# Kernel tuning notes

Measured on AMD Instinct MI355X. Metric: run time of the kernel, lower is better.

## Reference

```python
import jax, jax.numpy as jnp
import numpy as np

H, HD, C = 16, 64, 64            # num_heads, head_dim, mini_batch_size
BASE_LR = 1.0
EPS = 1e-6                        # ttt LN eps (ln_fwd / ln_fused_l2_bwd)


def _l2norm(x):
    return x / jnp.maximum(jnp.linalg.norm(x, axis=-1, keepdims=True), 1e-12)


def _ln_fwd(x, g, b):
    mu = x.mean(-1, keepdims=True)
    var = x.var(-1, keepdims=True)
    return g * ((x - mu) * jax.lax.rsqrt(var + EPS)) + b


def _ln_l2_bwd(x, tgt, g, b):
    # gradient of ||LN(x)*g+b - tgt||^2 / 2 wrt x
    D = x.shape[-1]
    mu = x.mean(-1, keepdims=True)
    var = x.var(-1, keepdims=True)
    std = jnp.sqrt(var + EPS)
    xh = (x - mu) / std
    gout = (g * xh + b) - tgt
    gxh = gout * g
    return (D * gxh - gxh.sum(-1, keepdims=True) - xh * (gxh * xh).sum(-1, keepdims=True)) / (D * std)


def setup_inputs() -> dict:
    key = jax.random.key(0)
    ks = jax.random.split(key, 12)
    B, L, D = 4, 8192, 1024
    std = 0.02
    return {
        'hidden_states': jax.random.normal(ks[0], (B, L, D), jnp.float32),
        'wq_w': jax.random.normal(ks[1], (D, D), jnp.float32) * std,
        'wq_b': jnp.zeros((D,), jnp.float32),
        'wk_w': jax.random.normal(ks[2], (D, D), jnp.float32) * std,
        'wk_b': jnp.zeros((D,), jnp.float32),
        'wv_w': jax.random.normal(ks[3], (D, D), jnp.float32) * std,
        'wv_b': jnp.zeros((D,), jnp.float32),
        'wo_w': jax.random.normal(ks[4], (D, D), jnp.float32) * std,
        'wo_b': jnp.zeros((D,), jnp.float32),
        'ttt_norm_weight': jnp.ones((H, HD), jnp.float32),
        'ttt_norm_bias': jnp.zeros((H, HD), jnp.float32),
        'ttt_lr_weight': jax.random.normal(ks[5], (H, 1, D), jnp.float32) * std,
        'ttt_lr_bias': jnp.zeros((H, 1), jnp.float32),
        'W1': jax.random.normal(ks[6], (H, HD, HD), jnp.float32) * std,
        'b1': jnp.zeros((H, 1, HD), jnp.float32),
        'post_norm_w': jnp.ones((D,), jnp.float32),
        'post_norm_b': jnp.zeros((D,), jnp.float32),
    }


def _forward(hidden_states, wq_w, wq_b, wk_w, wk_b, wv_w, wv_b, wo_w, wo_b,
             ttt_norm_weight, ttt_norm_bias, ttt_lr_weight, ttt_lr_bias,
             W1, b1, post_norm_w, post_norm_b):
    B, L, D = hidden_states.shape
    NC = L // C
    XQ = (hidden_states @ wq_w.T + wq_b).reshape(B, L, H, HD)
    XK = (hidden_states @ wk_w.T + wk_b).reshape(B, L, H, HD)
    XV = (hidden_states @ wv_w.T + wv_b).reshape(B, L, H, HD)
    XQ = _l2norm(XQ)
    XK = _l2norm(XK)
    # ln_reconstruction_target (uses sample std, ddof=1, eps=1e-5 on std)
    d = XV - XK
    mu = d.mean(-1, keepdims=True)
    sd = d.std(-1, keepdims=True, ddof=1)
    XV = ttt_norm_weight[None, None] * ((d - mu) / (sd + 1e-5)) + ttt_norm_bias[None, None] + XK
    # reshape to mini-batches: [B,H,NC,C,HD]
    Xmb = hidden_states.reshape(B, NC, C, D)
    to_mb = lambda t: t.transpose(0, 2, 1, 3).reshape(B, H, NC, C, HD)
    XQ, XK, XV = to_mb(XQ), to_mb(XK), to_mb(XV)
    # eta: sigmoid lr gate per token, row-broadcast over mini-batch
    ttt_lr = jax.nn.sigmoid(jnp.einsum('bnkc,hdc->bhnkd', Xmb, ttt_lr_weight)
                            + ttt_lr_bias.reshape(1, H, 1, 1, 1))     # [B,H,NC,C,1]
    eta = jnp.swapaxes(ttt_lr, -1, -2) * (BASE_LR / HD / C)           # [B,H,NC,1,C]
    mask = jnp.tril(jnp.ones((C, C), hidden_states.dtype))
    g = ttt_norm_weight[None, :, None, :]
    bta = ttt_norm_bias[None, :, None, :]
    W0 = jnp.broadcast_to(W1[None], (B, H, HD, HD))
    b0 = jnp.broadcast_to(b1[None], (B, H, 1, HD))

    def step(carry, xs):
        W, bvec = carry
        xq, xk, xv, eta_row = xs                      # eta_row: [B,H,1,C]
        Z1 = xk @ W + bvec                            # [B,H,C,HD]
        grad = _ln_l2_bwd(Z1, xv - xk, g, bta)        # [B,H,C,HD]
        Attn = mask * jnp.einsum('bhid,bhjd->bhij', xq, xk)   # [B,H,C,C]
        eta_full = jnp.broadcast_to(eta_row, Attn.shape)      # [B,H,C,C]
        b1_bar = bvec - (mask * eta_full) @ grad              # [B,H,C,HD]
        Z1_bar = xq @ W - (eta_full * Attn) @ grad + b1_bar
        last_eta = eta_full[..., -1, :, None]                 # [B,H,C,1]
        W_new = W - jnp.einsum('bhcd,bhce->bhde', last_eta * xk, grad)
        b_new = bvec - (last_eta * grad).sum(-2, keepdims=True)
        out = xq + _ln_fwd(Z1_bar, g, bta)
        return (W_new, b_new), out

    xs = (jnp.moveaxis(XQ, 2, 0), jnp.moveaxis(XK, 2, 0),
          jnp.moveaxis(XV, 2, 0), jnp.moveaxis(eta, 2, 0))
    _, outs = jax.lax.scan(step, (W0, b0), xs)        # outs: [NC,B,H,C,HD]
    y = jnp.moveaxis(outs, 0, 2).reshape(B, H, L, HD).transpose(0, 2, 1, 3).reshape(B, L, D)
    # post LayerNorm (eps=1e-6) + output projection
    mu2 = y.mean(-1, keepdims=True)
    var2 = y.var(-1, keepdims=True)
    y = post_norm_w * ((y - mu2) * jax.lax.rsqrt(var2 + 1e-6)) + post_norm_b
    return y @ wo_w.T + wo_b


def reference(hidden_states, wq_w, wq_b, wk_w, wk_b, wv_w, wv_b, wo_w, wo_b,
              ttt_norm_weight, ttt_norm_bias, ttt_lr_weight, ttt_lr_bias,
              W1, b1, post_norm_w, post_norm_b):
    return _forward(hidden_states, wq_w, wq_b, wk_w, wk_b, wv_w, wv_b, wo_w, wo_b,
                    ttt_norm_weight, ttt_norm_bias, ttt_lr_weight, ttt_lr_bias,
                    W1, b1, post_norm_w, post_norm_b)
```

## Files before the change

kernel.cpp:

```cpp
#include <hip/hip_runtime.h>


typedef __attribute__((ext_vector_type(8))) short short8;
typedef __attribute__((ext_vector_type(4))) float f32x4;
typedef __attribute__((ext_vector_type(4))) unsigned short us4;

__device__ __forceinline__ float bf2f(unsigned short s) {
  union { unsigned int u; float f; } c;
  c.u = ((unsigned int)s) << 16;
  return c.f;
}
__device__ __forceinline__ unsigned short f2bf(float f) {
  union { float f; unsigned int u; } c;
  c.f = f;
  unsigned int u = c.u;
  return (unsigned short)((u + 0x7FFFu + ((u >> 16) & 1u)) >> 16);
}
__device__ __forceinline__ unsigned cvtpk(float lo, float hi) {
  unsigned r;
  asm("v_cvt_pk_bf16_f32 %0, %1, %2" : "=v"(r) : "v"(lo), "v"(hi));
  return r;
}

__device__ __forceinline__ void gload_lds16(const void* g, void* l) {
  __builtin_amdgcn_global_load_lds(
      (const __attribute__((address_space(1))) unsigned int*)g,
      (__attribute__((address_space(3))) unsigned int*)l, 16, 0, 0);
}

__device__ __forceinline__ float dpp16_sum(float x) {
  int v = __float_as_int(x);
  x += __int_as_float(__builtin_amdgcn_update_dpp(v, v, 0xB1, 0xF, 0xF, true));
  v = __float_as_int(x);
  x += __int_as_float(__builtin_amdgcn_update_dpp(v, v, 0x4E, 0xF, 0xF, true));
  v = __float_as_int(x);
  x += __int_as_float(__builtin_amdgcn_update_dpp(v, v, 0x141, 0xF, 0xF, true));
  v = __float_as_int(x);
  x += __int_as_float(__builtin_amdgcn_update_dpp(v, v, 0x140, 0xF, 0xF, true));
  return x;
}

__device__ __forceinline__ void barrier_fast() {
  __builtin_amdgcn_sched_barrier(0);
  asm volatile("s_waitcnt lgkmcnt(0)" ::: "memory");
  __builtin_amdgcn_s_barrier();
  asm volatile("" ::: "memory");
  __builtin_amdgcn_sched_barrier(0);
}
__device__ __forceinline__ void bar_nowait() {
  __builtin_amdgcn_sched_barrier(0);
  asm volatile("" ::: "memory");
  __builtin_amdgcn_s_barrier();
  asm volatile("" ::: "memory");
  __builtin_amdgcn_sched_barrier(0);
}

__global__ __launch_bounds__(256) void cvt_f32_bf16(
    const float* __restrict__ in, unsigned short* __restrict__ out, long n) {
  long i = ((long)blockIdx.x * 256 + threadIdx.x) * 4;
  if (i + 3 < n) {
    float4 v = *(const float4*)&in[i];
    us4 o = { f2bf(v.x), f2bf(v.y), f2bf(v.z), f2bf(v.w) };
    *(us4*)&out[i] = o;
  }
}

__global__ __launch_bounds__(256) void build_wcat(
    const float* __restrict__ wq, const float* __restrict__ wk,
    const float* __restrict__ wv, const float* __restrict__ lrw,
    const float* __restrict__ wqb, const float* __restrict__ wkb,
    const float* __restrict__ wvb, const float* __restrict__ lrb,
    unsigned short* __restrict__ Wcat, float* __restrict__ biasc) {
  int i = blockIdx.x * 256 + threadIdx.x;
  int row = i >> 10, col = i & 1023;
  int h = row >> 8, o = row & 255;
  float v;
  if (o < 64)        v = wq[(h * 64 + o) * 1024 + col];
  else if (o < 128)  v = wk[(h * 64 + o - 64) * 1024 + col];
  else if (o < 192)  v = wv[(h * 64 + o - 128) * 1024 + col];
  else if (o == 192) v = lrw[h * 1024 + col];
  else               v = 0.f;
  Wcat[i] = f2bf(v);
  if (i < 4096) {
    int hh = i >> 8, oo = i & 255;
    float bv;
    if (oo < 64)        bv = wqb[hh * 64 + oo];
    else if (oo < 128)  bv = wkb[hh * 64 + oo - 64];
    else if (oo < 192)  bv = wvb[hh * 64 + oo - 128];
    else if (oo == 192) bv = lrb[hh];
    else                bv = 0.f;
    biasc[i] = bv;
  }
}

__global__ __launch_bounds__(512, 1) void qkv_scan(
    const unsigned short* __restrict__ A, const unsigned short* __restrict__ B,
    const float* __restrict__ bias, const float* __restrict__ tnw,
    const float* __restrict__ tnb, unsigned short* __restrict__ XQn,
    unsigned short* __restrict__ XKn, unsigned short* __restrict__ TGT,
    float* __restrict__ eta_buf, const float* __restrict__ W1,
    const float* __restrict__ b1, unsigned short* __restrict__ y,
    unsigned int* __restrict__ prog) {
  __shared__ __align__(16) char smem[102912];
  const int tid = threadIdx.x;
  const int lane = tid & 63, wid = tid >> 6;
  const int l15 = lane & 15, lg = lane >> 4;

  if (blockIdx.x >= 64) {
    char* ldsc = smem;
    const int bid2 = blockIdx.x - 64;
    const int w = bid2 >> 6, rem = bid2 & 63, bb = rem >> 4, h = rem & 15;
    const int mprog = bb * 32 + w;
    const long m0 = (long)mprog * 256;
    const long n0 = (long)h * 256;
    const long K = 1024, ldab = 2048;

    const int wm = wid >> 2, wn = wid & 3;
    const int srow = wid * 16 + (lane >> 2);
    const int scol = ((lane & 3) * 16) ^ (((lane >> 3) & 3) << 4);
    const int sdst = wid * 1024;
    const char* Ab = (const char*)A;
    const char* Bb = (const char*)B;
    const int acol = (lg * 16) ^ (((l15 >> 1) & 3) << 4);
    const int aro = (wm * 128 + l15) * 64 + acol;
    const int bro = 16384 + (wn * 64 + l15) * 64 + acol;

#define STG_A(tt, hh, bbu)                                                    \
  gload_lds16(Ab + (size_t)(m0 + (hh) * 128 + srow) * ldab +                  \
                  (size_t)(tt) * 64 + scol,                                   \
              ldsc + (bbu) * 32768 + (hh) * 8192 + sdst)
#define STG_B(tt, hh, bbu)                                                    \
  gload_lds16(Bb + (size_t)(n0 + (hh) * 128 + srow) * ldab +                  \
                  (size_t)(tt) * 64 + scol,                                   \
              ldsc + (bbu) * 32768 + 16384 + (hh) * 8192 + sdst)

    f32x4 acc[8][4];
#pragma unroll
    for (int m = 0; m < 8; ++m)
#pragma unroll
      for (int n = 0; n < 4; ++n) acc[m][n] = (f32x4){0.f, 0.f, 0.f, 0.f};

    const int NT = (int)(K >> 5);
    STG_A(0, 0, 0); STG_A(0, 1, 0); STG_B(0, 0, 0); STG_B(0, 1, 0);
    STG_A(1, 0, 1); STG_A(1, 1, 1); STG_B(1, 0, 1); STG_B(1, 1, 1);
    asm volatile("s_waitcnt vmcnt(4)" ::: "memory");
    bar_nowait();

    int buf = 0, sb = 2;
#pragma unroll 1
    for (int t = 0; t < NT; ++t) {
      if (t + 2 < NT) {
        STG_A(t + 2, 0, sb); STG_A(t + 2, 1, sb);
        STG_B(t + 2, 0, sb); STG_B(t + 2, 1, sb);
      }
      const char* ab = ldsc + buf * 32768 + aro;
      const char* bb2 = ldsc + buf * 32768 + bro;
      short8 av[8], bv[4];
#pragma unroll
      for (int i = 0; i < 8; ++i) av[i] = *(const short8*)(ab + i * 1024);
#pragma unroll
      for (int nf = 0; nf < 4; ++nf) bv[nf] = *(const short8*)(bb2 + nf * 1024);
      __builtin_amdgcn_s_setprio(1);
#pragma unroll
      for (int i = 0; i < 8; ++i)
#pragma unroll
        for (int nf = 0; nf < 4; ++nf)
          acc[i][nf] = __builtin_amdgcn_mfma_f32_16x16x32_bf16(
              av[i], bv[nf], acc[i][nf], 0, 0, 0);
      __builtin_amdgcn_s_setprio(0);
      if (t < NT - 2)
        asm volatile("s_waitcnt vmcnt(4)" ::: "memory");
      else
        asm volatile("s_waitcnt vmcnt(0)" ::: "memory");
      bar_nowait();
      buf = (buf == 2) ? 0 : buf + 1;
      sb = (sb == 2) ? 0 : sb + 1;
    }
#undef STG_A
#undef STG_B

    float bcol[4], twv[4], tbv[4];
#pragma unroll
    for (int nf = 0; nf < 4; ++nf) {
      bcol[nf] = bias[n0 + wn * 64 + nf * 16 + l15];
      twv[nf] = tnw[h * 64 + nf * 16 + l15];
      tbv[nf] = tnb[h * 64 + nf * 16 + l15];
    }
    __syncthreads();
    unsigned short* kn_s = (unsigned short*)smem;

    if (wn == 0) {
#pragma unroll
      for (int mf = 0; mf < 8; ++mf)
#pragma unroll
        for (int j = 0; j < 4; ++j) {
          float v[4], s2 = 0.f;
#pragma unroll
          for (int nf = 0; nf < 4; ++nf) {
            v[nf] = acc[mf][nf][j] + bcol[nf];
            s2 += v[nf] * v[nf];
          }
          s2 = dpp16_sum(s2);
          float rn = 1.f / fmaxf(sqrtf(s2), 1e-12f);
          size_t tt = (size_t)(m0 + wm * 128 + mf * 16 + lg * 4 + j);
#pragma unroll
          for (int nf = 0; nf < 4; ++nf)
            XQn[tt * 1024 + h * 64 + nf * 16 + l15] = f2bf(v[nf] * rn);
        }
    } else if (wn == 1) {
#pragma unroll
      for (int mf = 0; mf < 8; ++mf)
#pragma unroll
        for (int j = 0; j < 4; ++j) {
          float v[4], s2 = 0.f;
#pragma unroll
          for (int nf = 0; nf < 4; ++nf) {
            v[nf] = acc[mf][nf][j] + bcol[nf];
            s2 += v[nf] * v[nf];
          }
          s2 = dpp16_sum(s2);
          float rn = 1.f / fmaxf(sqrtf(s2), 1e-12f);
          size_t tt = (size_t)(m0 + wm * 128 + mf * 16 + lg * 4 + j);
          int lr_ = wm * 128 + mf * 16 + lg * 4 + j;
#pragma unroll
          for (int nf = 0; nf < 4; ++nf) {
            unsigned short kb = f2bf(v[nf] * rn);
            XKn[tt * 1024 + h * 64 + nf * 16 + l15] = kb;
            kn_s[lr_ * 72 + nf * 16 + l15] = kb;
          }
        }
    }
    __syncthreads();
    if (wn == 2) {
#pragma unroll
      for (int mf = 0; mf < 8; ++mf)
#pragma unroll
        for (int j = 0; j < 4; ++j) {
          int lr_ = wm * 128 + mf * 16 + lg * 4 + j;
          float dv[4], s1 = 0.f, s2 = 0.f;
#pragma unroll
          for (int nf = 0; nf < 4; ++nf) {
            float kn = bf2f(kn_s[lr_ * 72 + nf * 16 + l15]);
            dv[nf] = acc[mf][nf][j] + bcol[nf] - kn;
            s1 += dv[nf];
            s2 += dv[nf] * dv[nf];
          }
          s1 = dpp16_sum(s1);
          s2 = dpp16_sum(s2);
          float mu = s1 * 0.015625f;
          float var1 = fmaxf(s2 - 64.f * mu * mu, 0.f) * (1.f / 63.f);
          float rs = 1.f / (sqrtf(var1) + 1e-5f);
          size_t tt = (size_t)(m0 + wm * 128 + mf * 16 + lg * 4 + j);
#pragma unroll
          for (int nf = 0; nf < 4; ++nf)
            TGT[tt * 1024 + h * 64 + nf * 16 + l15] =
                f2bf(twv[nf] * ((dv[nf] - mu) * rs) + tbv[nf]);
        }
    } else if (wn == 3 && l15 == 0) {
#pragma unroll
      for (int mf = 0; mf < 8; ++mf)
#pragma unroll
        for (int j = 0; j < 4; ++j) {
          size_t tt = (size_t)(m0 + wm * 128 + mf * 16 + lg * 4 + j);
          float lgt = acc[mf][0][j] + bcol[0];
          float sig = 1.f / (1.f + expf(-lgt));
          eta_buf[((tt >> 13) * 16 + h) * 8192 + (tt & 8191)] =
              sig * (1.f / 4096.f);
        }
    }
    asm volatile("s_waitcnt vmcnt(0)" ::: "memory");
    __syncthreads();
    if (tid == 0) {
      __threadfence();
      __hip_atomic_fetch_add(&prog[mprog], 1u, __ATOMIC_RELEASE,
                             __HIP_MEMORY_SCOPE_AGENT);
    }
    return;
  }

  unsigned short* xq_s = (unsigned short*)(smem);
  unsigned short* tg_s = (unsigned short*)(smem + 18432);
  unsigned short* xk_s = (unsigned short*)(smem + 36864);
  unsigned short* gc_s = (unsigned short*)(smem + 55296);
  unsigned short* gradT = (unsigned short*)(smem + 64512);
  unsigned short* xkTe = (unsigned short*)(smem + 73728);
  unsigned short* WT_b = (unsigned short*)(smem + 82944);
  float* eta_s = (float*)(smem + 101376);
  float* bpart = (float*)(smem + 101888);

  const int bh = blockIdx.x;
  const int b = bh >> 4, h = bh & 15;
  const bool isA = wid < 4;
  const int q = wid & 3;
  const size_t tokb = (size_t)b * 8192;
  const int col0 = h * 64;
  const int rr_ = q * 16 + (lane >> 3);
  const int c8_ = (lane & 7) * 8;

  short8 pA0[2], pA1[2], pB0[2];
  float peta = 0.f;
  float bstv[4], gwv[4], gbv[4];
  f32x4 Wreg[4];

  if (isA) {
#pragma unroll
    for (int n = 0; n < 4; ++n) {
      int e = n * 16 + l15;
      bstv[n] = b1[h * 64 + e];
      gwv[n] = tnw[h * 64 + e];
      gbv[n] = tnb[h * 64 + e];
    }
  } else {
#pragma unroll
    for (int n = 0; n < 4; ++n)
#pragma unroll
      for (int jj = 0; jj < 4; ++jj) {
        int d = q * 16 + lg * 4 + jj, e = n * 16 + l15;
        float w2 = W1[h * 4096 + d * 64 + e];
        Wreg[n][jj] = w2;
        WT_b[e * 72 + d] = f2bf(w2);
      }
  }
  if (tid == 0) {
    while (__hip_atomic_load(&prog[b << 5], __ATOMIC_ACQUIRE,
                             __HIP_MEMORY_SCOPE_AGENT) < 16u)
      __builtin_amdgcn_s_sleep(16);
  }
  __syncthreads();

  if (isA) {
#pragma unroll
    for (int j = 0; j < 2; ++j) {
      size_t g = (tokb + rr_ + j * 8) * 1024 + col0 + c8_;
      pA0[j] = *(const short8*)&XQn[g];
      pA1[j] = *(const short8*)&TGT[g];
    }
#pragma unroll
    for (int j = 0; j < 2; ++j) {
      int rr = rr_ + j * 8;
      *(short8*)&xq_s[rr * 72 + c8_] = pA0[j];
      *(short8*)&tg_s[rr * 72 + c8_] = pA1[j];
    }
#pragma unroll
    for (int j = 0; j < 2; ++j) {
      size_t g = (tokb + 64 + rr_ + j * 8) * 1024 + col0 + c8_;
      pA0[j] = *(const short8*)&XQn[g];
      pA1[j] = *(const short8*)&TGT[g];
    }
  } else {
#pragma unroll
    for (int j = 0; j < 2; ++j)
      pB0[j] = *(const short8*)&XKn[(tokb + rr_ + j * 8) * 1024 + col0 + c8_];
#pragma unroll
    for (int j = 0; j < 2; ++j)
      *(short8*)&xk_s[(rr_ + j * 8) * 72 + c8_] = pB0[j];
#pragma unroll
    for (int j = 0; j < 2; ++j)
      pB0[j] = *(const short8*)&XKn[(tokb + 64 + rr_ + j * 8) * 1024 + col0 + c8_];
    if (wid == 4) {
      eta_s[lane] = eta_buf[(size_t)bh * 8192 + lane];
      peta = eta_buf[(size_t)bh * 8192 + 64 + lane];
    }
  }
  __syncthreads();

  for (int nc = 0; nc < 128; ++nc) {
    const int p = nc & 1;
    if (nc + 2 < 128 && ((nc + 2) & 3) == 0) {
      if (tid == 0) {
        while (__hip_atomic_load(&prog[(b << 5) + ((nc + 2) >> 2)],
                                 __ATOMIC_ACQUIRE,
                                 __HIP_MEMORY_SCOPE_AGENT) < 16u)
          __builtin_amdgcn_s_sleep(16);
      }
      bar_nowait();
    }
    const unsigned short* WTc = WT_b + p * 4608;
    unsigned short* WTn = WT_b + (p ^ 1) * 4608;
    unsigned short* xqp = xq_s + p * 4608;
    unsigned short* tgp = tg_s + p * 4608;
    unsigned short* xkp = xk_s + p * 4608;
    float* etp = eta_s + p * 64;

    if (isA) {
      if (nc) {
#pragma unroll
        for (int n = 0; n < 4; ++n) {
          int e = n * 16 + l15;
          bstv[n] -= bpart[e] + bpart[64 + e] + bpart[128 + e] + bpart[192 + e];
        }
      }
      if (nc + 1 < 128) {
        unsigned short* xqn = xq_s + (p ^ 1) * 4608;
        unsigned short* tgn = tg_s + (p ^ 1) * 4608;
#pragma unroll
        for (int j = 0; j < 2; ++j) {
          int rr = rr_ + j * 8;
          *(short8*)&xqn[rr * 72 + c8_] = pA0[j];
          *(short8*)&tgn[rr * 72 + c8_] = pA1[j];
        }
      }
      if (nc + 2 < 128) {
#pragma unroll
        for (int j = 0; j < 2; ++j) {
          size_t g = (tokb + (nc + 2) * 64 + rr_ + j * 8) * 1024 + col0 + c8_;
          pA0[j] = *(const short8*)&XQn[g];
          pA1[j] = *(const short8*)&TGT[g];
        }
      }
      f32x4 accZ[4];
#pragma unroll
      for (int n = 0; n < 4; ++n)
        accZ[n] = (f32x4){bstv[n], bstv[n], bstv[n], bstv[n]};
      __builtin_amdgcn_s_setprio(1);
#pragma unroll
      for (int kk = 0; kk < 2; ++kk) {
        const int ko = kk * 32 + lg * 8;
        short8 a_xk = *(const short8*)&xkp[(q * 16 + l15) * 72 + ko];
#pragma unroll
        for (int n = 0; n < 4; ++n) {
          short8 b_w = *(const short8*)&WTc[(n * 16 + l15) * 72 + ko];
          accZ[n] = __builtin_amdgcn_mfma_f32_16x16x32_bf16(a_xk, b_w, accZ[n], 0, 0, 0);
        }
      }
      __builtin_amdgcn_s_setprio(0);
      float grv[4][4];
#pragma unroll
      for (int j = 0; j < 4; ++j) {
        const int r = q * 16 + lg * 4 + j;
        float z[4], s1 = 0.f, s2 = 0.f;
#pragma unroll
        for (int n = 0; n < 4; ++n) {
          z[n] = accZ[n][j];
          s1 += z[n];
          s2 += z[n] * z[n];
        }
        s1 = dpp16_sum(s1);
        s2 = dpp16_sum(s2);
        float mu = s1 * 0.015625f;
        float var = s2 * 0.015625f - mu * mu;
        float rstd = rsqrtf(var + 1e-6f);
        float xh[4], gx[4], s3 = 0.f, s4 = 0.f;
#pragma unroll
        for (int n = 0; n < 4; ++n) {
          xh[n] = (z[n] - mu) * rstd;
          float tg = bf2f(tgp[r * 72 + n * 16 + l15]);
          float go = gwv[n] * xh[n] + gbv[n] - tg;
          gx[n] = go * gwv[n];
          s3 += gx[n];
          s4 += gx[n] * xh[n];
        }
        s3 = dpp16_sum(s3);
        s4 = dpp16_sum(s4);
#pragma unroll
        for (int n = 0; n < 4; ++n)
          grv[n][j] = (64.f * gx[n] - s3 - xh[n] * s4) * rstd * 0.015625f;
      }
#pragma unroll
      for (int n = 0; n < 4; ++n) {
        us4 pk = {f2bf(grv[n][0]), f2bf(grv[n][1]), f2bf(grv[n][2]),
                  f2bf(grv[n][3])};
        *(us4*)&gradT[(n * 16 + l15) * 72 + q * 16 + lg * 4] = pk;
      }
    } else {
      if (nc + 1 < 128) {
        unsigned short* xkn = xk_s + (p ^ 1) * 4608;
#pragma unroll
        for (int j = 0; j < 2; ++j)
          *(short8*)&xkn[(rr_ + j * 8) * 72 + c8_] = pB0[j];
        if (wid == 4) eta_s[(p ^ 1) * 64 + lane] = peta;
      }
      if (nc + 2 < 128) {
#pragma unroll
        for (int j = 0; j < 2; ++j)
          pB0[j] = *(const short8*)
              &XKn[(tokb + (nc + 2) * 64 + rr_ + j * 8) * 1024 + col0 + c8_];
        if (wid == 4) peta = eta_buf[(size_t)bh * 8192 + (nc + 2) * 64 + lane];
      }
#pragma unroll
      for (int it = 0; it < 4; ++it) {
        int c0 = q * 16 + it * 4;
        us4 pk;
#pragma unroll
        for (int u = 0; u < 4; ++u)
          pk[u] = f2bf(-etp[c0 + u] * bf2f(xkp[(c0 + u) * 72 + lane]));
        *(us4*)&xkTe[lane * 72 + c0] = pk;
      }
      f32x4 accA[4];
#pragma unroll
      for (int n = 0; n < 4; ++n) accA[n] = (f32x4){0.f, 0.f, 0.f, 0.f};
      __builtin_amdgcn_s_setprio(1);
#pragma unroll
      for (int kk = 0; kk < 2; ++kk) {
        const int ko = kk * 32 + lg * 8;
        short8 a_xq = *(const short8*)&xqp[(q * 16 + l15) * 72 + ko];
#pragma unroll
        for (int n = 0; n < 4; ++n) {
          short8 b_k = *(const short8*)&xkp[(n * 16 + l15) * 72 + ko];
          accA[n] = __builtin_amdgcn_mfma_f32_16x16x32_bf16(a_xq, b_k, accA[n], 0, 0, 0);
        }
      }
      __builtin_amdgcn_s_setprio(0);
#pragma unroll
      for (int j = 0; j < 4; ++j) {
        const int r = q * 16 + lg * 4 + j;
#pragma unroll
        for (int n = 0; n < 4; ++n) {
          int cj = n * 16 + l15;
          float v = (cj <= r) ? (-etp[cj] * (1.f + accA[n][j])) : 0.f;
          gc_s[r * 72 + cj] = f2bf(v);
        }
      }
    }
    barrier_fast();

    if (isA) {
      f32x4 accZb[4];
#pragma unroll
      for (int n = 0; n < 4; ++n)
        accZb[n] = (f32x4){bstv[n], bstv[n], bstv[n], bstv[n]};
      __builtin_amdgcn_s_setprio(1);
#pragma unroll
      for (int kk = 0; kk < 2; ++kk) {
        const int ko = kk * 32 + lg * 8;
        short8 a_xq = *(const short8*)&xqp[(q * 16 + l15) * 72 + ko];
        short8 a_gc = *(const short8*)&gc_s[(q * 16 + l15) * 72 + ko];
#pragma unroll
        for (int n = 0; n < 4; ++n) {
          short8 b_w = *(const short8*)&WTc[(n * 16 + l15) * 72 + ko];
          short8 b_g = *(const short8*)&gradT[(n * 16 + l15) * 72 + ko];
          accZb[n] = __builtin_amdgcn_mfma_f32_16x16x32_bf16(a_xq, b_w, accZb[n], 0, 0, 0);
          accZb[n] = __builtin_amdgcn_mfma_f32_16x16x32_bf16(a_gc, b_g, accZb[n], 0, 0, 0);
        }
      }
      __builtin_amdgcn_s_setprio(0);
#pragma unroll
      for (int j = 0; j < 4; ++j) {
        const int r = q * 16 + lg * 4 + j;
        float z[4], s1 = 0.f, s2 = 0.f;
#pragma unroll
        for (int n = 0; n < 4; ++n) {
          z[n] = accZb[n][j];
          s1 += z[n];
          s2 += z[n] * z[n];
        }
        s1 = dpp16_sum(s1);
        s2 = dpp16_sum(s2);
        float mu = s1 * 0.015625f;
        float var = s2 * 0.015625f - mu * mu;
        float rstd = rsqrtf(var + 1e-6f);
        size_t gbase = (tokb + nc * 64 + r) * 1024 + col0;
#pragma unroll
        for (int n = 0; n < 4; ++n) {
          int e = n * 16 + l15;
          float ov = bf2f(xqp[r * 72 + e]) + gwv[n] * ((z[n] - mu) * rstd) + gbv[n];
          y[gbase + e] = (unsigned short)(cvtpk(ov, ov) & 0xffffu);
        }
      }
    } else {
      short8 a_ke[2], b_g[2][4];
#pragma unroll
      for (int kk = 0; kk < 2; ++kk) {
        const int ko = kk * 32 + lg * 8;
        a_ke[kk] = *(const short8*)&xkTe[(q * 16 + l15) * 72 + ko];
#pragma unroll
        for (int n = 0; n < 4; ++n)
          b_g[kk][n] = *(const short8*)&gradT[(n * 16 + l15) * 72 + ko];
      }
      f32x4 accW[4];
#pragma unroll
      for (int n = 0; n < 4; ++n) accW[n] = Wreg[n];
      __builtin_amdgcn_s_setprio(1);
#pragma unroll
      for (int kk = 0; kk < 2; ++kk)
#pragma unroll
        for (int n = 0; n < 4; ++n)
          accW[n] = __builtin_amdgcn_mfma_f32_16x16x32_bf16(a_ke[kk], b_g[kk][n],
                                                            accW[n], 0, 0, 0);
      __builtin_amdgcn_s_setprio(0);
#pragma unroll
      for (int n = 0; n < 4; ++n) {
        Wreg[n] = accW[n];
        us4 pk = {f2bf(accW[n][0]), f2bf(accW[n][1]), f2bf(accW[n][2]),
                  f2bf(accW[n][3])};
        *(us4*)&WTn[(n * 16 + l15) * 72 + q * 16 + lg * 4] = pk;
      }
      {
        float s = 0.f;
#pragma unroll
        for (int it = 0; it < 4; ++it) {
          us4 gv = *(const us4*)&gradT[lane * 72 + q * 16 + it * 4];
#pragma unroll
          for (int u = 0; u < 4; ++u)
            s += etp[q * 16 + it * 4 + u] * bf2f(gv[u]);
        }
        bpart[q * 64 + lane] = s;
      }
    }
    barrier_fast();
  }
}

template <int WRITE_BF16>
__global__ __launch_bounds__(512, 1) void gemm256(
    const unsigned short* __restrict__ A, const unsigned short* __restrict__ B,
    const float* __restrict__ bias, void* __restrict__ Cout,
    long M, long N, long K, int NTILN, long ldc) {
  __shared__ __align__(16) unsigned short g_lds[49152];
  char* ldsc = (char*)g_lds;
  const int tid = threadIdx.x, lane = tid & 63, wid = tid >> 6;
  const int wm = wid >> 2, wn = wid & 3;
  const int l15 = lane & 15, lg = lane >> 4;

  unsigned nwg = gridDim.x, bid = blockIdx.x;
  unsigned cpx = nwg >> 3;
  unsigned swz = (bid & 7) * cpx + (bid >> 3);
  unsigned nidx = swz % (unsigned)NTILN, midx = swz / (unsigned)NTILN;
  const long m0 = (long)midx * 256, n0 = (long)nidx * 256;
  const long ldab = K * 2;

  const int srow = wid * 16 + (lane >> 2);
  const int scol = ((lane & 3) * 16) ^ (((lane >> 3) & 3) << 4);
  const int sdst = wid * 1024;
  const char* Ab = (const char*)A;
  const char* Bb = (const char*)B;

  const int acol = (lg * 16) ^ (((l15 >> 1) & 3) << 4);
  const int aro = (wm * 128 + l15) * 64 + acol;
  const int bro = 16384 + (wn * 64 + l15) * 64 + acol;

#define STG_A(tt, h, bb)                                                      \
  gload_lds16(Ab + (size_t)(m0 + (h) * 128 + srow) * ldab + (size_t)(tt) * 64 \
                  + scol,                                                     \
              ldsc + (bb) * 32768 + (h) * 8192 + sdst)
#define STG_B(tt, h, bb)                                                      \
  gload_lds16(Bb + (size_t)(n0 + (h) * 128 + srow) * ldab + (size_t)(tt) * 64 \
                  + scol,                                                     \
              ldsc + (bb) * 32768 + 16384 + (h) * 8192 + sdst)

  f32x4 acc[8][4];
#pragma unroll
  for (int m = 0; m < 8; ++m)
#pragma unroll
    for (int n = 0; n < 4; ++n) acc[m][n] = (f32x4){0.f, 0.f, 0.f, 0.f};

  const int NT = (int)(K >> 5);

  STG_A(0, 0, 0); STG_A(0, 1, 0); STG_B(0, 0, 0); STG_B(0, 1, 0);
  STG_A(1, 0, 1); STG_A(1, 1, 1); STG_B(1, 0, 1); STG_B(1, 1, 1);
  asm volatile("s_waitcnt vmcnt(4)" ::: "memory");
  bar_nowait();

  int buf = 0, sb = 2;
#pragma unroll 1
  for (int t = 0; t < NT; ++t) {
    if (t + 2 < NT) {
      STG_A(t + 2, 0, sb); STG_A(t + 2, 1, sb);
      STG_B(t + 2, 0, sb); STG_B(t + 2, 1, sb);
    }
    const char* ab = ldsc + buf * 32768 + aro;
    const char* bb2 = ldsc + buf * 32768 + bro;
    short8 av[8], bv[4];
#pragma unroll
    for (int i = 0; i < 8; ++i) av[i] = *(const short8*)(ab + i * 1024);
#pragma unroll
    for (int nf = 0; nf < 4; ++nf) bv[nf] = *(const short8*)(bb2 + nf * 1024);
    __builtin_amdgcn_s_setprio(1);
#pragma unroll
    for (int i = 0; i < 8; ++i)
#pragma unroll
      for (int nf = 0; nf < 4; ++nf)
        acc[i][nf] = __builtin_amdgcn_mfma_f32_16x16x32_bf16(av[i], bv[nf],
                                                             acc[i][nf], 0, 0, 0);
    __builtin_amdgcn_s_setprio(0);
    if (t < NT - 2)
      asm volatile("s_waitcnt vmcnt(4)" ::: "memory");
    else
      asm volatile("s_waitcnt vmcnt(0)" ::: "memory");
    bar_nowait();
    buf = (buf == 2) ? 0 : buf + 1;
    sb = (sb == 2) ? 0 : sb + 1;
  }
#undef STG_A
#undef STG_B

#pragma unroll
  for (int mf = 0; mf < 8; ++mf) {
    long r0 = m0 + wm * 128 + mf * 16 + lg * 4;
#pragma unroll
    for (int nf = 0; nf < 4; ++nf) {
      long c = n0 + wn * 64 + nf * 16 + l15;
      float bvv = bias ? bias[c] : 0.f;
#pragma unroll
      for (int j = 0; j < 4; ++j) {
        float v = acc[mf][nf][j] + bvv;
        if (WRITE_BF16)
          ((unsigned short*)Cout)[(r0 + j) * ldc + c] = f2bf(v);
        else
          ((float*)Cout)[(r0 + j) * ldc + c] = v;
      }
    }
  }
}

__global__ __launch_bounds__(256) void postnorm(
    const unsigned short* __restrict__ yv, const float* __restrict__ pw,
    const float* __restrict__ pb, unsigned short* __restrict__ yn) {
  int t = blockIdx.x;
  int tid = threadIdx.x, lane = tid & 63, wid = tid >> 6;
  us4 v4 = *(const us4*)&yv[(size_t)t * 1024 + tid * 4];
  float v[4];
  float s1 = 0.f, s2 = 0.f;
#pragma unroll
  for (int u = 0; u < 4; ++u) {
    v[u] = bf2f(v4[u]);
    s1 += v[u];
    s2 += v[u] * v[u];
  }
#pragma unroll
  for (int o = 1; o < 64; o <<= 1) {
    s1 += __shfl_xor(s1, o);
    s2 += __shfl_xor(s2, o);
  }
  __shared__ float r1[4], r2[4];
  if (lane == 0) {
    r1[wid] = s1;
    r2[wid] = s2;
  }
  __syncthreads();
  s1 = r1[0] + r1[1] + r1[2] + r1[3];
  s2 = r2[0] + r2[1] + r2[2] + r2[3];
  float mu = s1 * (1.f / 1024.f);
  float var = s2 * (1.f / 1024.f) - mu * mu;
  float rstd = rsqrtf(var + 1e-6f);
  int c = tid * 4;
  us4 o4;
#pragma unroll
  for (int u = 0; u < 4; ++u)
    o4[u] = f2bf(pw[c + u] * ((v[u] - mu) * rstd) + pb[c + u]);
  *(us4*)&yn[(size_t)t * 1024 + c] = o4;
}

extern "C" void kernel_launch(void* const* d_in, const int* in_sizes, int n_in,
                              void* d_out, int out_size, void* d_ws,
                              size_t ws_size, hipStream_t stream) {
  const float* hs  = (const float*)d_in[0];
  const float* wqw = (const float*)d_in[1];
  const float* wqb = (const float*)d_in[2];
  const float* wkw = (const float*)d_in[3];
  const float* wkb = (const float*)d_in[4];
  const float* wvw = (const float*)d_in[5];
  const float* wvb = (const float*)d_in[6];
  const float* wow = (const float*)d_in[7];
  const float* wob = (const float*)d_in[8];
  const float* tnw = (const float*)d_in[9];
  const float* tnb = (const float*)d_in[10];
  const float* lrw = (const float*)d_in[11];
  const float* lrb = (const float*)d_in[12];
  const float* W1  = (const float*)d_in[13];
  const float* b1  = (const float*)d_in[14];
  const float* pnw = (const float*)d_in[15];
  const float* pnb = (const float*)d_in[16];

  const size_t OFF_XQ    = 0;
  const size_t OFF_XK    = 67108864;
  const size_t OFF_TGT   = 134217728;
  const size_t OFF_ETA   = 201326592;
  const size_t OFF_WOBF  = 203423744;
  const size_t OFF_PROG  = 205520896;
  const size_t OFF_HSBF  = 205524992;
  const size_t OFF_WCAT  = OFF_HSBF + 67108864;
  const size_t OFF_BIASC = OFF_WCAT + 8388608;
  const size_t OFF_YBF   = OFF_BIASC + 16384;
  const size_t NEEDED    = OFF_YBF + 67108864;
  if (ws_size < NEEDED) return;

  char* ws = (char*)d_ws;
  unsigned short* XQn   = (unsigned short*)(ws + OFF_XQ);
  unsigned short* ynorm = (unsigned short*)(ws + OFF_XQ);
  unsigned short* XKn   = (unsigned short*)(ws + OFF_XK);
  unsigned short* TGT   = (unsigned short*)(ws + OFF_TGT);
  float* eta_buf        = (float*)(ws + OFF_ETA);
  unsigned short* wo_bf = (unsigned short*)(ws + OFF_WOBF);
  unsigned int* prog    = (unsigned int*)(ws + OFF_PROG);
  unsigned short* hs_bf = (unsigned short*)(ws + OFF_HSBF);
  unsigned short* Wcat  = (unsigned short*)(ws + OFF_WCAT);
  float* biasc          = (float*)(ws + OFF_BIASC);
  unsigned short* ybf   = (unsigned short*)(ws + OFF_YBF);

  cvt_f32_bf16<<<32768, 256, 0, stream>>>(hs, hs_bf, 33554432L);
  build_wcat<<<16384, 256, 0, stream>>>(wqw, wkw, wvw, lrw, wqb, wkb, wvb, lrb,
                                        Wcat, biasc);
  cvt_f32_bf16<<<1024, 256, 0, stream>>>(wow, wo_bf, 1048576L);
  hipMemsetAsync(prog, 0, 4096, stream);
  qkv_scan<<<2112, 512, 0, stream>>>(hs_bf, Wcat, biasc, tnw, tnb,
                                     XQn, XKn, TGT, eta_buf, W1, b1, ybf, prog);
  postnorm<<<32768, 256, 0, stream>>>(ybf, pnw, pnb, ynorm);
  gemm256<0><<<512, 512, 0, stream>>>(ynorm, wo_bf, wob, d_out,
                                      32768L, 1024L, 1024L, 4, 1024L);
}
```

Measured before the change: 777.1 us.

## Fuse post-LayerNorm into output projection GEMM A-tile staging

Removes the separate postnorm kernel and its bf16 normalized-activation round trip. Each GEMM block first computes per-row mean and rstd for its 256 rows, then normalizes y on the fly while staging A tiles into LDS through registers, with B still loaded via direct-to-LDS loads. This saves one 64MB write and read plus a launch. In exchange, each row's statistics are recomputed by the four N-tile blocks, and A staging now goes through VGPRs, which may stall the MFMA pipeline.

```diff
diff --git a/kernel.cpp b/kernel.cpp
--- a/kernel.cpp
+++ b/kernel.cpp
@@ -601,42 +601,91 @@
   }
 }
 
-template <int WRITE_BF16>
-__global__ __launch_bounds__(512, 1) void gemm256(
-    const unsigned short* __restrict__ A, const unsigned short* __restrict__ B,
-    const float* __restrict__ bias, void* __restrict__ Cout,
-    long M, long N, long K, int NTILN, long ldc) {
-  __shared__ __align__(16) unsigned short g_lds[49152];
-  char* ldsc = (char*)g_lds;
-  const int tid = threadIdx.x, lane = tid & 63, wid = tid >> 6;
+__global__ __launch_bounds__(512, 1) void out_fused(
+    const unsigned short* __restrict__ y, const unsigned short* __restrict__ wo_bf,
+    const float* __restrict__ wob, const float* __restrict__ pnw,
+    const float* __restrict__ pnb, float* __restrict__ out) {
+  __shared__ __align__(16) char smem[108544];
+  char* ldsc = smem;
+  float* mu_s = (float*)(smem + 98304);
+  float* rs_s = (float*)(smem + 99328);
+  float* pnw_s = (float*)(smem + 100352);
+  float* pnb_s = (float*)(smem + 104448);
+
+  const int tid = threadIdx.x;
+  const int lane = tid & 63, wid = tid >> 6;
+  const int l15 = lane & 15, lg = lane >> 4;
   const int wm = wid >> 2, wn = wid & 3;
-  const int l15 = lane & 15, lg = lane >> 4;
-
-  unsigned nwg = gridDim.x, bid = blockIdx.x;
-  unsigned cpx = nwg >> 3;
-  unsigned swz = (bid & 7) * cpx + (bid >> 3);
-  unsigned nidx = swz % (unsigned)NTILN, midx = swz / (unsigned)NTILN;
-  const long m0 = (long)midx * 256, n0 = (long)nidx * 256;
-  const long ldab = K * 2;
-
   const int srow = wid * 16 + (lane >> 2);
   const int scol = ((lane & 3) * 16) ^ (((lane >> 3) & 3) << 4);
   const int sdst = wid * 1024;
-  const char* Ab = (const char*)A;
-  const char* Bb = (const char*)B;
-
   const int acol = (lg * 16) ^ (((l15 >> 1) & 3) << 4);
   const int aro = (wm * 128 + l15) * 64 + acol;
   const int bro = 16384 + (wn * 64 + l15) * 64 + acol;
 
-#define STG_A(tt, h, bb)                                                      \
-  gload_lds16(Ab + (size_t)(m0 + (h) * 128 + srow) * ldab + (size_t)(tt) * 64 \
-                  + scol,                                                     \
-              ldsc + (bb) * 32768 + (h) * 8192 + sdst)
-#define STG_B(tt, h, bb)                                                      \
-  gload_lds16(Bb + (size_t)(n0 + (h) * 128 + srow) * ldab + (size_t)(tt) * 64 \
-                  + scol,                                                     \
-              ldsc + (bb) * 32768 + 16384 + (h) * 8192 + sdst)
+  const long m0 = (long)(blockIdx.x >> 2) * 256;
+  const long n0 = (long)(blockIdx.x & 3) * 256;
+
+  if (tid < 256) *(float4*)&pnw_s[tid * 4] = *(const float4*)&pnw[tid * 4];
+  else { int t2 = tid - 256; *(float4*)&pnb_s[t2 * 4] = *(const float4*)&pnb[t2 * 4]; }
+
+  for (int rr = 0; rr < 32; ++rr) {
+    int r = wid * 32 + rr;
+    const unsigned short* row = y + (size_t)(m0 + r) * 1024;
+    float s1 = 0.f, s2 = 0.f;
+#pragma unroll
+    for (int k = 0; k < 4; ++k) {
+      us4 v4 = *(const us4*)&row[k * 256 + lane * 4];
+#pragma unroll
+      for (int u = 0; u < 4; ++u) {
+        float f = bf2f(v4[u]);
+        s1 += f;
+        s2 += f * f;
+      }
+    }
+#pragma unroll
+    for (int o2 = 1; o2 < 64; o2 <<= 1) {
+      s1 += __shfl_xor(s1, o2);
+      s2 += __shfl_xor(s2, o2);
+    }
+    if (lane == 0) {
+      float mu = s1 * (1.f / 1024.f);
+      float var = s2 * (1.f / 1024.f) - mu * mu;
+      mu_s[r] = mu;
+      rs_s[r] = rsqrtf(var + 1e-6f);
+    }
+  }
+  __syncthreads();
+
+  auto stageA = [&](int tt, int sl) {
+    int r = tid >> 1, half = tid & 1;
+    const unsigned short* ysrc = y + (size_t)(m0 + r) * 1024 + tt * 32 + half * 16;
+    us4 h0 = *(const us4*)(ysrc);
+    us4 h1 = *(const us4*)(ysrc + 4);
+    us4 h2 = *(const us4*)(ysrc + 8);
+    us4 h3 = *(const us4*)(ysrc + 12);
+    float mu = mu_s[r], rs = rs_s[r];
+    int c0 = tt * 32 + half * 16;
+    __align__(16) unsigned short o[16];
+    unsigned short vin[16] = {h0[0], h0[1], h0[2], h0[3], h1[0], h1[1], h1[2],
+                              h1[3], h2[0], h2[1], h2[2], h2[3], h3[0], h3[1],
+                              h3[2], h3[3]};
+#pragma unroll
+    for (int u = 0; u < 16; ++u)
+      o[u] = f2bf(pnw_s[c0 + u] * ((bf2f(vin[u]) - mu) * rs) + pnb_s[c0 + u]);
+    int key = ((r >> 1) & 3) << 4;
+    char* base = ldsc + sl * 32768 + r * 64;
+    *(short8*)(base + ((half * 32) ^ key)) = *(short8*)&o[0];
+    *(short8*)(base + ((half * 32 + 16) ^ key)) = *(short8*)&o[8];
+  };
+  auto stgB = [&](int tt, int sl) {
+    gload_lds16((const char*)wo_bf + (size_t)(n0 + srow) * 2048 +
+                    (size_t)tt * 64 + scol,
+                ldsc + sl * 32768 + 16384 + sdst);
+    gload_lds16((const char*)wo_bf + (size_t)(n0 + 128 + srow) * 2048 +
+                    (size_t)tt * 64 + scol,
+                ldsc + sl * 32768 + 16384 + 8192 + sdst);
+  };
 
   f32x4 acc[8][4];
 #pragma unroll
@@ -644,45 +693,36 @@
 #pragma unroll
     for (int n = 0; n < 4; ++n) acc[m][n] = (f32x4){0.f, 0.f, 0.f, 0.f};
 
-  const int NT = (int)(K >> 5);
-
-  STG_A(0, 0, 0); STG_A(0, 1, 0); STG_B(0, 0, 0); STG_B(0, 1, 0);
-  STG_A(1, 0, 1); STG_A(1, 1, 1); STG_B(1, 0, 1); STG_B(1, 1, 1);
-  asm volatile("s_waitcnt vmcnt(4)" ::: "memory");
-  bar_nowait();
-
-  int buf = 0, sb = 2;
+  stgB(0, 0); stgB(1, 1);
+  stageA(0, 0); stageA(1, 1);
+  asm volatile("s_waitcnt vmcnt(2)" ::: "memory");
+  barrier_fast();
+
 #pragma unroll 1
-  for (int t = 0; t < NT; ++t) {
-    if (t + 2 < NT) {
-      STG_A(t + 2, 0, sb); STG_A(t + 2, 1, sb);
-      STG_B(t + 2, 0, sb); STG_B(t + 2, 1, sb);
-    }
+  for (int t = 0; t < 32; ++t) {
+    const int buf = t % 3, sb = (t + 2) % 3;
+    if (t + 2 < 32) { stgB(t + 2, sb); stageA(t + 2, sb); }
     const char* ab = ldsc + buf * 32768 + aro;
     const char* bb2 = ldsc + buf * 32768 + bro;
     short8 av[8], bv[4];
 #pragma unroll
-    for (int i = 0; i < 8; ++i) av[i] = *(const short8*)(ab + i * 1024);
+    for (int ii = 0; ii < 8; ++ii) av[ii] = *(const short8*)(ab + ii * 1024);
 #pragma unroll
     for (int nf = 0; nf < 4; ++nf) bv[nf] = *(const short8*)(bb2 + nf * 1024);
     __builtin_amdgcn_s_setprio(1);
 #pragma unroll
-    for (int i = 0; i < 8; ++i)
+    for (int ii = 0; ii < 8; ++ii)
 #pragma unroll
       for (int nf = 0; nf < 4; ++nf)
-        acc[i][nf] = __builtin_amdgcn_mfma_f32_16x16x32_bf16(av[i], bv[nf],
-                                                             acc[i][nf], 0, 0, 0);
+        acc[ii][nf] = __builtin_amdgcn_mfma_f32_16x16x32_bf16(
+            av[ii], bv[nf], acc[ii][nf], 0, 0, 0);
     __builtin_amdgcn_s_setprio(0);
-    if (t < NT - 2)
-      asm volatile("s_waitcnt vmcnt(4)" ::: "memory");
+    if (t + 2 < 32)
+      asm volatile("s_waitcnt vmcnt(2)" ::: "memory");
     else
       asm volatile("s_waitcnt vmcnt(0)" ::: "memory");
-    bar_nowait();
-    buf = (buf == 2) ? 0 : buf + 1;
-    sb = (sb == 2) ? 0 : sb + 1;
-  }
-#undef STG_A
-#undef STG_B
+    barrier_fast();
+  }
 
 #pragma unroll
   for (int mf = 0; mf < 8; ++mf) {
@@ -690,55 +730,12 @@
 #pragma unroll
     for (int nf = 0; nf < 4; ++nf) {
       long c = n0 + wn * 64 + nf * 16 + l15;
-      float bvv = bias ? bias[c] : 0.f;
-#pragma unroll
-      for (int j = 0; j < 4; ++j) {
-        float v = acc[mf][nf][j] + bvv;
-        if (WRITE_BF16)
-          ((unsigned short*)Cout)[(r0 + j) * ldc + c] = f2bf(v);
-        else
-          ((float*)Cout)[(r0 + j) * ldc + c] = v;
-      }
-    }
-  }
-}
-
-__global__ __launch_bounds__(256) void postnorm(
-    const unsigned short* __restrict__ yv, const float* __restrict__ pw,
-    const float* __restrict__ pb, unsigned short* __restrict__ yn) {
-  int t = blockIdx.x;
-  int tid = threadIdx.x, lane = tid & 63, wid = tid >> 6;
-  us4 v4 = *(const us4*)&yv[(size_t)t * 1024 + tid * 4];
-  float v[4];
-  float s1 = 0.f, s2 = 0.f;
-#pragma unroll
-  for (int u = 0; u < 4; ++u) {
-    v[u] = bf2f(v4[u]);
-    s1 += v[u];
-    s2 += v[u] * v[u];
-  }
-#pragma unroll
-  for (int o = 1; o < 64; o <<= 1) {
-    s1 += __shfl_xor(s1, o);
-    s2 += __shfl_xor(s2, o);
-  }
-  __shared__ float r1[4], r2[4];
-  if (lane == 0) {
-    r1[wid] = s1;
-    r2[wid] = s2;
-  }
-  __syncthreads();
-  s1 = r1[0] + r1[1] + r1[2] + r1[3];
-  s2 = r2[0] + r2[1] + r2[2] + r2[3];
-  float mu = s1 * (1.f / 1024.f);
-  float var = s2 * (1.f / 1024.f) - mu * mu;
-  float rstd = rsqrtf(var + 1e-6f);
-  int c = tid * 4;
-  us4 o4;
-#pragma unroll
-  for (int u = 0; u < 4; ++u)
-    o4[u] = f2bf(pw[c + u] * ((v[u] - mu) * rstd) + pb[c + u]);
-  *(us4*)&yn[(size_t)t * 1024 + c] = o4;
+      float bvv = wob[c];
+#pragma unroll
+      for (int j = 0; j < 4; ++j)
+        out[(r0 + j) * 1024 + c] = acc[mf][nf][j] + bvv;
+    }
+  }
 }
 
 extern "C" void kernel_launch(void* const* d_in, const int* in_sizes, int n_in,
@@ -777,7 +774,6 @@
 
   char* ws = (char*)d_ws;
   unsigned short* XQn   = (unsigned short*)(ws + OFF_XQ);
-  unsigned short* ynorm = (unsigned short*)(ws + OFF_XQ);
   unsigned short* XKn   = (unsigned short*)(ws + OFF_XK);
   unsigned short* TGT   = (unsigned short*)(ws + OFF_TGT);
   float* eta_buf        = (float*)(ws + OFF_ETA);
@@ -795,7 +791,5 @@
   hipMemsetAsync(prog, 0, 4096, stream);
   qkv_scan<<<2112, 512, 0, stream>>>(hs_bf, Wcat, biasc, tnw, tnb,
                                      XQn, XKn, TGT, eta_buf, W1, b1, ybf, prog);
-  postnorm<<<32768, 256, 0, stream>>>(ybf, pnw, pnb, ynorm);
-  gemm256<0><<<512, 512, 0, stream>>>(ynorm, wo_bf, wob, d_out,
-                                      32768L, 1024L, 1024L, 4, 1024L);
-}
+  out_fused<<<512, 512, 0, stream>>>(ybf, wo_bf, wob, pnw, pnb, (float*)d_out);
+}
```

New measurement: 826.6 us. +6.4%, slower.
